# Optimization experiments

Hardware: AMD Instinct MI355X
Metric: run time of the kernel (lower is better)

The kernel has to match this reference:

```python
import jax, jax.numpy as jnp
import numpy as np

B, T, I, H, FC, O = 256, 4096, 63, 50, 64, 2


def setup_inputs() -> dict:
    key = jax.random.key(0)
    ks = jax.random.split(key, 9)
    s_ih = 1.0 / np.sqrt(H)
    inp = {
        "x": jax.random.normal(ks[0], (B, T, I), dtype=jnp.float32),
        # RNN params (PyTorch layout: W_ih [H, I], W_hh [H, H])
        "W_ih": jax.random.uniform(ks[1], (H, I), jnp.float32, -s_ih, s_ih),
        "b_ih": jax.random.uniform(ks[2], (H,), jnp.float32, -s_ih, s_ih),
        "W_hh": jax.random.uniform(ks[3], (H, H), jnp.float32, -s_ih, s_ih),
        "b_hh": jax.random.uniform(ks[4], (H,), jnp.float32, -s_ih, s_ih),
        # MLP head
        "W1": jax.random.uniform(ks[5], (FC, H), jnp.float32, -1.0 / np.sqrt(H), 1.0 / np.sqrt(H)),
        "b1": jax.random.uniform(ks[6], (FC,), jnp.float32, -1.0 / np.sqrt(H), 1.0 / np.sqrt(H)),
        "W2": jax.random.uniform(ks[7], (O, FC), jnp.float32, -1.0 / np.sqrt(FC), 1.0 / np.sqrt(FC)),
        "b2": jax.random.uniform(ks[8], (O,), jnp.float32, -1.0 / np.sqrt(FC), 1.0 / np.sqrt(FC)),
    }
    return inp


def reference(x, W_ih, b_ih, W_hh, b_hh, W1, b1, W2, b2):
    # Precompute input projection for all timesteps in one GEMM: [B, T, H]
    xz = jnp.einsum("bti,hi->bth", x, W_ih) + b_ih
    h0 = jnp.zeros((x.shape[0], W_hh.shape[0]), x.dtype)

    def step(h, xt):  # h: [B, H], xt: [B, H]
        h_new = jnp.tanh(xt + h @ W_hh.T + b_hh)
        return h_new, None

    # scan over time; only the final hidden state is needed (out[:, -1, :])
    hT, _ = jax.lax.scan(step, h0, jnp.swapaxes(xz, 0, 1))
    out = jax.nn.relu(hT @ W1.T + b1) @ W2.T + b2  # [B, O]
    probs = jax.nn.softmax(out, axis=1)
    return jnp.argmax(probs, axis=1).astype(jnp.float32)  # [B]
```

## Files before the change

### kernel.cpp

```cpp
#include <hip/hip_runtime.h>
#include <cstdint>
#include <cstddef>

#define BB 256
#define TT 4096
#define ID 63
#define HH 50
#define FCD 64

typedef float f32x2 __attribute__((ext_vector_type(2)));

__device__ __forceinline__ uint32_t rl_u32(float v, int lane) {
    return (uint32_t)__builtin_amdgcn_readlane(__float_as_int(v), lane);
}
__device__ __forceinline__ float rl_f(float v, int lane) {
    return __int_as_float(__builtin_amdgcn_readlane(__float_as_int(v), lane));
}

__device__ __forceinline__ f32x2 pk_mul(uint64_t hp, f32x2 w) {
    f32x2 d;
    asm("v_pk_mul_f32 %0, %1, %2" : "=v"(d) : "s"(hp), "v"(w));
    return d;
}
__device__ __forceinline__ void pk_fma(f32x2& acc, uint64_t hp, f32x2 w) {
    asm("v_pk_fma_f32 %0, %1, %2, %0" : "+v"(acc) : "s"(hp), "v"(w));
}

__device__ __forceinline__ float fast_tanh(float x) {
    float e = __builtin_amdgcn_exp2f(x * 2.88539008177792681472f);
    return 1.0f - 2.0f * __builtin_amdgcn_rcpf(e + 1.0f);
}

__global__ __launch_bounds__(64) void proj_kernel(
    const float* __restrict__ x, const float* __restrict__ W_ih,
    const float* __restrict__ b_ih, const float* __restrict__ b_hh,
    float* __restrict__ z)
{
    __shared__ float xs[64 * ID];
    const int lane = threadIdx.x;
    const int64_t row0 = (int64_t)blockIdx.x * 64;

    const float4* __restrict__ xin4 = (const float4*)(x + row0 * ID);
    float4* xs4 = (float4*)xs;
    for (int i = lane; i < (64 * ID) / 4; i += 64) xs4[i] = xin4[i];
    __syncthreads();

    float xr[ID];
#pragma unroll
    for (int i = 0; i < ID; ++i) xr[i] = xs[lane * ID + i];
    __syncthreads();

    float* zs = xs;
#pragma unroll 1
    for (int j = 0; j < HH; ++j) {
        const float* __restrict__ wp = W_ih + j * ID;
        float a0 = b_ih[j] + b_hh[j], a1 = 0.f, a2 = 0.f, a3 = 0.f;
#pragma unroll
        for (int i = 0; i < 60; i += 4) {
            a0 = fmaf(xr[i + 0], wp[i + 0], a0);
            a1 = fmaf(xr[i + 1], wp[i + 1], a1);
            a2 = fmaf(xr[i + 2], wp[i + 2], a2);
            a3 = fmaf(xr[i + 3], wp[i + 3], a3);
        }
        a0 = fmaf(xr[60], wp[60], a0);
        a1 = fmaf(xr[61], wp[61], a1);
        a2 = fmaf(xr[62], wp[62], a2);
        zs[lane * HH + j] = (a0 + a2) + (a1 + a3);
    }
    __syncthreads();

    const float2* zs2 = (const float2*)zs;
    float2* __restrict__ zo2 = (float2*)(z + row0 * HH);
#pragma unroll
    for (int i = lane; i < (64 * HH) / 2; i += 64) zo2[i] = zs2[i];
}

__global__ __launch_bounds__(64) void rnn_kernel(
    const float* __restrict__ z, const float* __restrict__ W_hh,
    const float* __restrict__ W1, const float* __restrict__ b1,
    const float* __restrict__ W2, const float* __restrict__ b2,
    float* __restrict__ out)
{
    const int b = blockIdx.x;
    const int lane = threadIdx.x;
    const int j = (lane < HH) ? lane : (HH - 1);

    f32x2 wpk[25];
#pragma unroll
    for (int k = 0; k < 25; ++k) {
        wpk[k].x = W_hh[j * HH + 2 * k];
        wpk[k].y = W_hh[j * HH + 2 * k + 1];
    }

    const float* __restrict__ base = z + (int64_t)b * TT * HH;
    const int col = j;

    float zp[8], zn[8];
#pragma unroll
    for (int u = 0; u < 8; ++u) zp[u] = base[u * HH + col];
    const float* p = base + 8 * HH;

    float vh = 0.f;
    for (int t0 = 0; t0 < TT; t0 += 8) {
        if (t0 + 8 < TT) {
#pragma unroll
            for (int u = 0; u < 8; ++u) zn[u] = p[u * HH + col];
        }
        p += 8 * HH;
#pragma unroll
        for (int u = 0; u < 8; ++u) {
            uint64_t hp[25];
#pragma unroll
            for (int k = 0; k < 25; ++k) {
                uint32_t lo = rl_u32(vh, 2 * k);
                uint32_t hi = rl_u32(vh, 2 * k + 1);
                hp[k] = (uint64_t)lo | ((uint64_t)hi << 32);
            }
            f32x2 accA = pk_mul(hp[0], wpk[0]);
            f32x2 accB = pk_mul(hp[1], wpk[1]);
#pragma unroll
            for (int k = 2; k < 25; k += 2) pk_fma(accA, hp[k], wpk[k]);
#pragma unroll
            for (int k = 3; k < 25; k += 2) pk_fma(accB, hp[k], wpk[k]);
            f32x2 ab = accA + accB;
            float s = zp[u] + (ab.x + ab.y);
            vh = fast_tanh(s);
        }
#pragma unroll
        for (int u = 0; u < 8; ++u) zp[u] = zn[u];
    }

    float f = b1[lane];
#pragma unroll
    for (int k = 0; k < HH; ++k) f = fmaf(rl_f(vh, k), W1[lane * HH + k], f);
    f = fmaxf(f, 0.f);
    float p0 = f * W2[lane];
    float p1 = f * W2[FCD + lane];
#pragma unroll
    for (int off = 32; off > 0; off >>= 1) {
        p0 += __shfl_down(p0, off, 64);
        p1 += __shfl_down(p1, off, 64);
    }
    if (lane == 0) out[b] = ((p1 + b2[1]) > (p0 + b2[0])) ? 1.0f : 0.0f;
}

__global__ __launch_bounds__(64) void rnn_fused_kernel(
    const float* __restrict__ x, const float* __restrict__ W_ih,
    const float* __restrict__ b_ih, const float* __restrict__ W_hh,
    const float* __restrict__ b_hh, const float* __restrict__ W1,
    const float* __restrict__ b1, const float* __restrict__ W2,
    const float* __restrict__ b2, float* __restrict__ out)
{
    const int b = blockIdx.x;
    const int lane = threadIdx.x;
    const int j = (lane < HH) ? lane : (HH - 1);

    float whh[HH];
#pragma unroll
    for (int k = 0; k < HH; ++k) whh[k] = W_hh[j * HH + k];
    float wih[ID];
#pragma unroll
    for (int i = 0; i < ID; ++i) wih[i] = W_ih[j * ID + i];
    const float bias = b_ih[j] + b_hh[j];

    const float* __restrict__ base = x + (int64_t)b * TT * ID;
    const int col = (lane < ID) ? lane : (ID - 1);

    float zp[8], zn[8];
#pragma unroll
    for (int u = 0; u < 8; ++u) zp[u] = base[u * ID + col];

    float vh = 0.f;
    for (int t0 = 0; t0 < TT; t0 += 8) {
        if (t0 + 8 < TT) {
#pragma unroll
            for (int u = 0; u < 8; ++u) zn[u] = base[(int64_t)(t0 + 8 + u) * ID + col];
        }
#pragma unroll
        for (int u = 0; u < 8; ++u) {
            float a0 = bias, a1 = 0.f, a2 = 0.f, a3 = 0.f;
#pragma unroll
            for (int i = 0; i < 60; i += 4) {
                a0 = fmaf(rl_f(zp[u], i + 0), wih[i + 0], a0);
                a1 = fmaf(rl_f(zp[u], i + 1), wih[i + 1], a1);
                a2 = fmaf(rl_f(zp[u], i + 2), wih[i + 2], a2);
                a3 = fmaf(rl_f(zp[u], i + 3), wih[i + 3], a3);
            }
            a0 = fmaf(rl_f(zp[u], 60), wih[60], a0);
            a1 = fmaf(rl_f(zp[u], 61), wih[61], a1);
            a2 = fmaf(rl_f(zp[u], 62), wih[62], a2);
#pragma unroll
            for (int k = 0; k < 48; k += 4) {
                a0 = fmaf(rl_f(vh, k + 0), whh[k + 0], a0);
                a1 = fmaf(rl_f(vh, k + 1), whh[k + 1], a1);
                a2 = fmaf(rl_f(vh, k + 2), whh[k + 2], a2);
                a3 = fmaf(rl_f(vh, k + 3), whh[k + 3], a3);
            }
            a0 = fmaf(rl_f(vh, 48), whh[48], a0);
            a1 = fmaf(rl_f(vh, 49), whh[49], a1);
            vh = fast_tanh((a0 + a2) + (a1 + a3));
        }
#pragma unroll
        for (int u = 0; u < 8; ++u) zp[u] = zn[u];
    }

    float f = b1[lane];
#pragma unroll
    for (int k = 0; k < HH; ++k) f = fmaf(rl_f(vh, k), W1[lane * HH + k], f);
    f = fmaxf(f, 0.f);
    float p0 = f * W2[lane];
    float p1 = f * W2[FCD + lane];
#pragma unroll
    for (int off = 32; off > 0; off >>= 1) {
        p0 += __shfl_down(p0, off, 64);
        p1 += __shfl_down(p1, off, 64);
    }
    if (lane == 0) out[b] = ((p1 + b2[1]) > (p0 + b2[0])) ? 1.0f : 0.0f;
}

extern "C" void kernel_launch(void* const* d_in, const int* in_sizes, int n_in,
                              void* d_out, int out_size, void* d_ws, size_t ws_size,
                              hipStream_t stream)
{
    const float* x    = (const float*)d_in[0];
    const float* W_ih = (const float*)d_in[1];
    const float* b_ih = (const float*)d_in[2];
    const float* W_hh = (const float*)d_in[3];
    const float* b_hh = (const float*)d_in[4];
    const float* W1   = (const float*)d_in[5];
    const float* b1   = (const float*)d_in[6];
    const float* W2   = (const float*)d_in[7];
    const float* b2   = (const float*)d_in[8];
    float* out = (float*)d_out;

    const size_t zbytes = (size_t)BB * TT * HH * sizeof(float);
    if (ws_size >= zbytes) {
        float* z = (float*)d_ws;
        proj_kernel<<<(BB * TT) / 64, 64, 0, stream>>>(x, W_ih, b_ih, b_hh, z);
        rnn_kernel<<<BB, 64, 0, stream>>>(z, W_hh, W1, b1, W2, b2, out);
    } else {
        rnn_fused_kernel<<<BB, 64, 0, stream>>>(x, W_ih, b_ih, W_hh, b_hh,
                                                W1, b1, W2, b2, out);
    }
}
```

Before: 1.360 ms.

## Interleave two batch recurrences per wave and pair output columns in projection

The RNN kernel now has each 64-lane wave run two batch rows. The readlane broadcasts of one sequence's hidden state are interleaved with the packed FMAs of the other sequence, hiding the serial readlane-to-FMA latency of the recurrence. The grid is halved, so only 128 waves run on a GPU with many CUs, and each wave carries more registers. The projection kernel also computes two output columns per loop iteration so each loaded x value is reused twice.

```diff
diff --git a/kernel.cpp b/kernel.cpp
--- a/kernel.cpp
+++ b/kernel.cpp
@@ -15,6 +15,11 @@
 }
 __device__ __forceinline__ float rl_f(float v, int lane) {
     return __int_as_float(__builtin_amdgcn_readlane(__float_as_int(v), lane));
+}
+__device__ __forceinline__ uint64_t rlpair(float v, int kk) {
+    uint32_t lo = rl_u32(v, 2 * kk);
+    uint32_t hi = rl_u32(v, 2 * kk + 1);
+    return (uint64_t)lo | ((uint64_t)hi << 32);
 }
 
 __device__ __forceinline__ f32x2 pk_mul(uint64_t hp, f32x2 w) {
@@ -52,20 +57,30 @@
 
     float* zs = xs;
 #pragma unroll 1
-    for (int j = 0; j < HH; ++j) {
-        const float* __restrict__ wp = W_ih + j * ID;
-        float a0 = b_ih[j] + b_hh[j], a1 = 0.f, a2 = 0.f, a3 = 0.f;
+    for (int j = 0; j < HH; j += 2) {
+        const float* __restrict__ w0 = W_ih + j * ID;
+        const float* __restrict__ w1 = w0 + ID;
+        float a0 = b_ih[j] + b_hh[j],         a1 = 0.f, a2 = 0.f, a3 = 0.f;
+        float c0 = b_ih[j + 1] + b_hh[j + 1], c1 = 0.f, c2 = 0.f, c3 = 0.f;
 #pragma unroll
         for (int i = 0; i < 60; i += 4) {
-            a0 = fmaf(xr[i + 0], wp[i + 0], a0);
-            a1 = fmaf(xr[i + 1], wp[i + 1], a1);
-            a2 = fmaf(xr[i + 2], wp[i + 2], a2);
-            a3 = fmaf(xr[i + 3], wp[i + 3], a3);
-        }
-        a0 = fmaf(xr[60], wp[60], a0);
-        a1 = fmaf(xr[61], wp[61], a1);
-        a2 = fmaf(xr[62], wp[62], a2);
-        zs[lane * HH + j] = (a0 + a2) + (a1 + a3);
+            a0 = fmaf(xr[i + 0], w0[i + 0], a0);
+            a1 = fmaf(xr[i + 1], w0[i + 1], a1);
+            a2 = fmaf(xr[i + 2], w0[i + 2], a2);
+            a3 = fmaf(xr[i + 3], w0[i + 3], a3);
+            c0 = fmaf(xr[i + 0], w1[i + 0], c0);
+            c1 = fmaf(xr[i + 1], w1[i + 1], c1);
+            c2 = fmaf(xr[i + 2], w1[i + 2], c2);
+            c3 = fmaf(xr[i + 3], w1[i + 3], c3);
+        }
+        a0 = fmaf(xr[60], w0[60], a0);
+        a1 = fmaf(xr[61], w0[61], a1);
+        a2 = fmaf(xr[62], w0[62], a2);
+        c0 = fmaf(xr[60], w1[60], c0);
+        c1 = fmaf(xr[61], w1[61], c1);
+        c2 = fmaf(xr[62], w1[62], c2);
+        zs[lane * HH + j]     = (a0 + a2) + (a1 + a3);
+        zs[lane * HH + j + 1] = (c0 + c2) + (c1 + c3);
     }
     __syncthreads();
 
@@ -81,7 +96,8 @@
     const float* __restrict__ W2, const float* __restrict__ b2,
     float* __restrict__ out)
 {
-    const int b = blockIdx.x;
+    const int blk = blockIdx.x;
+    const int bA = 2 * blk, bB = 2 * blk + 1;
     const int lane = threadIdx.x;
     const int j = (lane < HH) ? lane : (HH - 1);
 
@@ -92,56 +108,98 @@
         wpk[k].y = W_hh[j * HH + 2 * k + 1];
     }
 
-    const float* __restrict__ base = z + (int64_t)b * TT * HH;
+    const float* __restrict__ baseA = z + (int64_t)bA * TT * HH;
+    const float* __restrict__ baseB = z + (int64_t)bB * TT * HH;
     const int col = j;
 
-    float zp[8], zn[8];
-#pragma unroll
-    for (int u = 0; u < 8; ++u) zp[u] = base[u * HH + col];
-    const float* p = base + 8 * HH;
-
-    float vh = 0.f;
+    float zpA[8], znA[8], zpB[8], znB[8];
+#pragma unroll
+    for (int u = 0; u < 8; ++u) {
+        zpA[u] = baseA[u * HH + col];
+        zpB[u] = baseB[u * HH + col];
+    }
+    const float* pA = baseA + 8 * HH;
+    const float* pB = baseB + 8 * HH;
+
+    float vhA = 0.f, vhB = 0.f;
+    uint64_t hpA[25], hpB[25];
+#pragma unroll
+    for (int k = 0; k < 25; ++k) hpB[k] = 0;
+
     for (int t0 = 0; t0 < TT; t0 += 8) {
         if (t0 + 8 < TT) {
 #pragma unroll
-            for (int u = 0; u < 8; ++u) zn[u] = p[u * HH + col];
-        }
-        p += 8 * HH;
+            for (int u = 0; u < 8; ++u) {
+                znA[u] = pA[u * HH + col];
+                znB[u] = pB[u * HH + col];
+            }
+        }
+        pA += 8 * HH;
+        pB += 8 * HH;
 #pragma unroll
         for (int u = 0; u < 8; ++u) {
-            uint64_t hp[25];
-#pragma unroll
-            for (int k = 0; k < 25; ++k) {
-                uint32_t lo = rl_u32(vh, 2 * k);
-                uint32_t hi = rl_u32(vh, 2 * k + 1);
-                hp[k] = (uint64_t)lo | ((uint64_t)hi << 32);
-            }
-            f32x2 accA = pk_mul(hp[0], wpk[0]);
-            f32x2 accB = pk_mul(hp[1], wpk[1]);
-#pragma unroll
-            for (int k = 2; k < 25; k += 2) pk_fma(accA, hp[k], wpk[k]);
-#pragma unroll
-            for (int k = 3; k < 25; k += 2) pk_fma(accB, hp[k], wpk[k]);
-            f32x2 ab = accA + accB;
-            float s = zp[u] + (ab.x + ab.y);
-            vh = fast_tanh(s);
-        }
-#pragma unroll
-        for (int u = 0; u < 8; ++u) zp[u] = zn[u];
-    }
-
-    float f = b1[lane];
-#pragma unroll
-    for (int k = 0; k < HH; ++k) f = fmaf(rl_f(vh, k), W1[lane * HH + k], f);
-    f = fmaxf(f, 0.f);
-    float p0 = f * W2[lane];
-    float p1 = f * W2[FCD + lane];
+            {
+                f32x2 a0 = pk_mul(hpB[0], wpk[0]);
+                f32x2 a1 = pk_mul(hpB[1], wpk[1]);
+                pk_fma(a0, hpB[2], wpk[2]);
+                pk_fma(a1, hpB[3], wpk[3]);
+#pragma unroll
+                for (int kk = 0; kk < 21; ++kk) {
+                    hpA[kk] = rlpair(vhA, kk);
+                    const int m = kk + 4;
+                    if (m & 1) pk_fma(a1, hpB[m], wpk[m]);
+                    else       pk_fma(a0, hpB[m], wpk[m]);
+                }
+#pragma unroll
+                for (int kk = 21; kk < 25; ++kk) hpA[kk] = rlpair(vhA, kk);
+                f32x2 ab = a0 + a1;
+                vhB = fast_tanh(zpB[u] + (ab.x + ab.y));
+            }
+            {
+                f32x2 a0 = pk_mul(hpA[0], wpk[0]);
+                f32x2 a1 = pk_mul(hpA[1], wpk[1]);
+                pk_fma(a0, hpA[2], wpk[2]);
+                pk_fma(a1, hpA[3], wpk[3]);
+#pragma unroll
+                for (int kk = 0; kk < 21; ++kk) {
+                    hpB[kk] = rlpair(vhB, kk);
+                    const int m = kk + 4;
+                    if (m & 1) pk_fma(a1, hpA[m], wpk[m]);
+                    else       pk_fma(a0, hpA[m], wpk[m]);
+                }
+#pragma unroll
+                for (int kk = 21; kk < 25; ++kk) hpB[kk] = rlpair(vhB, kk);
+                f32x2 ab = a0 + a1;
+                vhA = fast_tanh(zpA[u] + (ab.x + ab.y));
+            }
+        }
+#pragma unroll
+        for (int u = 0; u < 8; ++u) { zpA[u] = znA[u]; zpB[u] = znB[u]; }
+    }
+
+    float fA = b1[lane];
+    float fB = b1[lane];
+#pragma unroll
+    for (int k = 0; k < HH; ++k) {
+        const float w1v = W1[lane * HH + k];
+        fA = fmaf(rl_f(vhA, k), w1v, fA);
+        fB = fmaf(rl_f(vhB, k), w1v, fB);
+    }
+    fA = fmaxf(fA, 0.f);
+    fB = fmaxf(fB, 0.f);
+    float p0A = fA * W2[lane], p1A = fA * W2[FCD + lane];
+    float p0B = fB * W2[lane], p1B = fB * W2[FCD + lane];
 #pragma unroll
     for (int off = 32; off > 0; off >>= 1) {
-        p0 += __shfl_down(p0, off, 64);
-        p1 += __shfl_down(p1, off, 64);
-    }
-    if (lane == 0) out[b] = ((p1 + b2[1]) > (p0 + b2[0])) ? 1.0f : 0.0f;
+        p0A += __shfl_down(p0A, off, 64);
+        p1A += __shfl_down(p1A, off, 64);
+        p0B += __shfl_down(p0B, off, 64);
+        p1B += __shfl_down(p1B, off, 64);
+    }
+    if (lane == 0) {
+        out[bA] = ((p1A + b2[1]) > (p0A + b2[0])) ? 1.0f : 0.0f;
+        out[bB] = ((p1B + b2[1]) > (p0B + b2[0])) ? 1.0f : 0.0f;
+    }
 }
 
 __global__ __launch_bounds__(64) void rnn_fused_kernel(
@@ -237,7 +295,7 @@
     if (ws_size >= zbytes) {
         float* z = (float*)d_ws;
         proj_kernel<<<(BB * TT) / 64, 64, 0, stream>>>(x, W_ih, b_ih, b_hh, z);
-        rnn_kernel<<<BB, 64, 0, stream>>>(z, W_hh, W1, b1, W2, b2, out);
+        rnn_kernel<<<BB / 2, 64, 0, stream>>>(z, W_hh, W1, b1, W2, b2, out);
     } else {
         rnn_fused_kernel<<<BB, 64, 0, stream>>>(x, W_ih, b_ih, W_hh, b_hh,
                                                 W1, b1, W2, b2, out);
```

New measurement: 2.152 ms. +58.2%, slower.
